# Kernel optimization log

Hardware: AMD Instinct MI355X
Metric: run time of the kernel (lower is better)

The kernel has to match this reference:

```python
import jax, jax.numpy as jnp
import numpy as np

N_EMBD = 1024
N_HEAD = 16
HEAD_DIM = N_EMBD // N_HEAD


def setup_inputs() -> dict:
    key = jax.random.key(0)
    k1, k2, k3, k4, k5 = jax.random.split(key, 5)
    x = jax.random.normal(k1, (4, 2048, N_EMBD), dtype=jnp.float32)
    s = 1.0 / np.sqrt(N_EMBD)
    W_attn = jax.random.normal(k2, (N_EMBD, 3 * N_EMBD), dtype=jnp.float32) * s
    b_attn = jnp.zeros((3 * N_EMBD,), dtype=jnp.float32)
    W_proj = jax.random.normal(k3, (N_EMBD, N_EMBD), dtype=jnp.float32) * s
    b_proj = jnp.zeros((N_EMBD,), dtype=jnp.float32)
    return {"x": x, "W_attn": W_attn, "b_attn": b_attn, "W_proj": W_proj, "b_proj": b_proj}


def _attention(x, W_attn, b_attn, W_proj, b_proj):
    B, T, C = x.shape
    qkv = jnp.einsum("btc,cd->btd", x, W_attn) + b_attn  # [B,T,3C]
    q, k, v = jnp.split(qkv, 3, axis=-1)
    # [B,T,C] -> [B,H,T,D]
    def heads(t):
        return t.reshape(B, T, N_HEAD, HEAD_DIM).transpose(0, 2, 1, 3)
    q, k, v = heads(q), heads(k), heads(v)
    scale = 1.0 / np.sqrt(HEAD_DIM)
    scores = jnp.einsum("bhqd,bhkd->bhqk", q, k) * scale  # [B,H,T,T]
    causal = jnp.tril(jnp.ones((T, T), dtype=bool))
    scores = jnp.where(causal, scores, jnp.finfo(scores.dtype).min)
    attn = jax.nn.softmax(scores, axis=-1)
    y = jnp.einsum("bhqk,bhkd->bhqd", attn, v)  # [B,H,T,D]
    y = y.transpose(0, 2, 1, 3).reshape(B, T, C)
    return jnp.einsum("btc,cd->btd", y, W_proj) + b_proj


def reference(x, W_attn, b_attn, W_proj, b_proj):
    return _attention(x, W_attn, b_attn, W_proj, b_proj)
```

## Files before the change

kernel.cpp:

```cpp
#include <hip/hip_runtime.h>
#include <hip/hip_bf16.h>

#define BB 4
#define TT 2048
#define CC 1024
#define HH 16
#define DD 64
#define BT (BB*TT)
#define C3 (3*CC)
#define LDST 72
#define QSCALE 0.18033688011112042f

typedef __attribute__((ext_vector_type(8))) short short8;
typedef __attribute__((ext_vector_type(4))) float f32x4;

__device__ __forceinline__ short f2bs(float f) {
  __hip_bfloat16 h = __float2bfloat16(f);
  return *reinterpret_cast<short*>(&h);
}

__device__ __forceinline__ void gl_lds16(const short* g, short* l) {
  __builtin_amdgcn_global_load_lds(
      (const __attribute__((address_space(1))) void*)(g),
      (__attribute__((address_space(3))) void*)(l), 16, 0, 0);
}

__global__ __launch_bounds__(256)
void prep(const float* __restrict__ Wa, short* __restrict__ Wat,
          const float* __restrict__ Wp, short* __restrict__ Wpt,
          const float* __restrict__ x, short* __restrict__ Xb)
{
  __shared__ float Lt[64][65];
  const int bx = blockIdx.x;
  if (bx >= 64) {
    size_t chunk = (size_t)(bx - 64) * 16 + blockIdx.y;
    size_t i = (chunk * 256 + threadIdx.x) * 8;
    float4 a = *reinterpret_cast<const float4*>(x + i);
    float4 b = *reinterpret_cast<const float4*>(x + i + 4);
    short8 o;
    o[0] = f2bs(a.x); o[1] = f2bs(a.y); o[2] = f2bs(a.z); o[3] = f2bs(a.w);
    o[4] = f2bs(b.x); o[5] = f2bs(b.y); o[6] = f2bs(b.z); o[7] = f2bs(b.w);
    *reinterpret_cast<short8*>(Xb + i) = o;
    return;
  }
  const bool isA = (bx < 48);
  const float* in  = isA ? Wa  : Wp;
  short*       out = isA ? Wat : Wpt;
  const int N  = isA ? C3 : CC;
  const int n0 = (isA ? bx : bx - 48) * 64;
  const int k0 = blockIdx.y * 64;
  const int cx = threadIdx.x & 15, rr = threadIdx.x >> 4;
#pragma unroll
  for (int p = 0; p < 4; ++p) {
    int kr = p * 16 + rr;
    float4 u = *reinterpret_cast<const float4*>(in + (size_t)(k0 + kr) * N + n0 + cx * 4);
    Lt[kr][cx * 4 + 0] = u.x;
    Lt[kr][cx * 4 + 1] = u.y;
    Lt[kr][cx * 4 + 2] = u.z;
    Lt[kr][cx * 4 + 3] = u.w;
  }
  __syncthreads();
#pragma unroll
  for (int p = 0; p < 4; ++p) {
    int nr = p * 16 + rr;
    short4 o;
    o.x = f2bs(Lt[cx * 4 + 0][nr]);
    o.y = f2bs(Lt[cx * 4 + 1][nr]);
    o.z = f2bs(Lt[cx * 4 + 2][nr]);
    o.w = f2bs(Lt[cx * 4 + 3][nr]);
    *reinterpret_cast<short4*>(out + (size_t)(n0 + nr) * CC + k0 + cx * 4) = o;
  }
}

template<bool QKV>
__global__ __launch_bounds__(512, 2)
void gemm256(const short* __restrict__ A, const short* __restrict__ Bt,
             const float* __restrict__ bias,
             short* __restrict__ qb, short* __restrict__ kb, short* __restrict__ vb,
             float* __restrict__ out)
{
  __shared__ __align__(16) short As[2][2 * 256 * 32];
  __shared__ __align__(16) short Bs[2][2 * 256 * 32];

  const int t = threadIdx.x;
  const int lane = t & 63;
  const int l16 = lane & 15, quad = lane >> 4;
  const int w = t >> 6;
  const int wr = w >> 2, wc = w & 3;

  const int per   = gridDim.x >> 3;
  const int chunk = (blockIdx.x & 7) * per + (blockIdx.x >> 3);
  const int NBC   = QKV ? 12 : 4;
  const int brow  = chunk / NBC, bcol = chunk % NBC;
  const int row0  = brow * 256;
  const int col0  = bcol * 256;

  auto stageHalf = [&](int b, int kc, int ktile) {
#pragma unroll
    for (int q = 0; q < 2; ++q) {
      int gq = (w * 2 + q) * 64 + lane;
      int rq = gq >> 2;
      int cs = ((gq & 3) ^ (rq & 3)) << 3;
      gl_lds16(A  + (size_t)(row0 + rq) * CC + ktile * 64 + kc * 32 + cs,
               &As[b][kc * 8192 + gq * 8]);
      gl_lds16(Bt + (size_t)(col0 + rq) * CC + ktile * 64 + kc * 32 + cs,
               &Bs[b][kc * 8192 + gq * 8]);
    }
  };

  f32x4 acc[8][4];
#pragma unroll
  for (int i = 0; i < 8; ++i)
#pragma unroll
    for (int j = 0; j < 4; ++j) acc[i][j] = (f32x4){0.f, 0.f, 0.f, 0.f};

  stageHalf(0, 0, 0);
  stageHalf(0, 1, 0);

  for (int kt = 0; kt < 16; ++kt) {
    const int cur = kt & 1;
    const short* Ac = As[cur];
    const short* Bc = Bs[cur];
#pragma unroll
    for (int kc = 0; kc < 2; ++kc) {
      if (kt == 15 && kc == 1) {
        asm volatile("s_waitcnt vmcnt(0)" ::: "memory");
      } else {
        asm volatile("s_waitcnt vmcnt(4)" ::: "memory");
      }
      __builtin_amdgcn_s_barrier();
      __builtin_amdgcn_sched_barrier(0);

      short8 af[8], bf[4];
#pragma unroll
      for (int j = 0; j < 4; ++j) {
        int rb = wc * 64 + j * 16 + l16;
        bf[j] = *reinterpret_cast<const short8*>(
            &Bc[kc * 8192 + rb * 32 + (((quad ^ rb) & 3) << 3)]);
      }
#pragma unroll
      for (int i = 0; i < 8; ++i) {
        int ra = wr * 128 + i * 16 + l16;
        af[i] = *reinterpret_cast<const short8*>(
            &Ac[kc * 8192 + ra * 32 + (((quad ^ ra) & 3) << 3)]);
      }

      if (kt < 15) stageHalf(cur ^ 1, kc, kt + 1);

      __builtin_amdgcn_s_setprio(1);
#pragma unroll
      for (int i = 0; i < 8; ++i)
#pragma unroll
        for (int j = 0; j < 4; ++j)
          acc[i][j] = __builtin_amdgcn_mfma_f32_16x16x32_bf16(af[i], bf[j], acc[i][j], 0, 0, 0);
      __builtin_amdgcn_s_setprio(0);
    }
  }

  if constexpr (QKV) {
#pragma unroll
    for (int j = 0; j < 4; ++j) {
      int colb = col0 + wc * 64 + j * 16 + l16;
      int sel  = colb >> 10, cin = colb & 1023;
      int h    = cin >> 6,  dd  = cin & 63;
      float bv = bias[colb];
#pragma unroll
      for (int i = 0; i < 8; ++i)
#pragma unroll
        for (int r = 0; r < 4; ++r) {
          int row = row0 + wr * 128 + i * 16 + quad * 4 + r;
          int bi = row >> 11, tt = row & 2047;
          float val = acc[i][j][r] + bv;
          size_t hb = (size_t)(bi * HH + h);
          if (sel == 0) {
            qb[(hb * TT + tt) * DD + dd] = f2bs(val * QSCALE);
          } else if (sel == 1) {
            kb[(hb * TT + tt) * DD + dd] = f2bs(val);
          } else {
            int tp = (tt & ~63) | (((tt & 15) << 2) | ((tt >> 4) & 3));
            vb[(hb * DD + dd) * TT + tp] = f2bs(val);
          }
        }
    }
  } else {
#pragma unroll
    for (int j = 0; j < 4; ++j) {
      int col = col0 + wc * 64 + j * 16 + l16;
      float bv = bias[col];
#pragma unroll
      for (int i = 0; i < 8; ++i)
#pragma unroll
        for (int r = 0; r < 4; ++r) {
          int row = row0 + wr * 128 + i * 16 + quad * 4 + r;
          out[(size_t)row * CC + col] = acc[i][j][r] + bv;
        }
    }
  }
}

__global__ __launch_bounds__(256, 4)
void attn_mfma(const short* __restrict__ Qb, const short* __restrict__ Kb,
               const short* __restrict__ Vb, short* __restrict__ Y)
{
  __shared__ __align__(16) short Ks[64 * LDST];
  __shared__ __align__(16) short Vt[64 * LDST];
  __shared__ __align__(16) short Pw[4 * 16 * LDST];

  const int t    = threadIdx.x;
  const int w    = t >> 6;
  const int lane = t & 63;
  const int l16  = lane & 15;
  const int quad = lane >> 4;

  const int linear = blockIdx.x + 16 * (blockIdx.y + 16 * blockIdx.z);
  const int nb  = (linear & 7) * 128 + (linear >> 3);
  const int qt0 = nb & 15;
  const int h   = (nb >> 4) & 15;
  const int bi  = nb >> 8;
  const size_t head = (size_t)(bi * HH + h) * TT * DD;

  short* myP = &Pw[w * 16 * LDST];
  const int sr = t >> 2;
  const int sc = (t & 3) << 4;

  const int qts[2] = { qt0, 31 - qt0 };

#pragma unroll
  for (int half = 0; half < 2; ++half) {
    const int qt = qts[half];
    const int q0 = qt * 64;

    short8 qf[2];
#pragma unroll
    for (int kc = 0; kc < 2; ++kc)
      qf[kc] = *reinterpret_cast<const short8*>(
          &Qb[head + (size_t)(q0 + w * 16 + l16) * DD + kc * 32 + quad * 8]);

    f32x4 O[4];
#pragma unroll
    for (int dt = 0; dt < 4; ++dt) O[dt] = (f32x4){0.f, 0.f, 0.f, 0.f};
    float lsum[4] = {};

    for (int kt = 0; kt <= qt; ++kt) {
      const int k0 = kt * 64;
      __syncthreads();

      {
        const short* kg = Kb + head + (size_t)(k0 + sr) * DD + sc;
        short8 a = *reinterpret_cast<const short8*>(kg);
        short8 b = *reinterpret_cast<const short8*>(kg + 8);
        *reinterpret_cast<short8*>(&Ks[sr * LDST + sc])     = a;
        *reinterpret_cast<short8*>(&Ks[sr * LDST + sc + 8]) = b;
        const short* vg = Vb + head + (size_t)sr * TT + k0 + sc;
        short8 c = *reinterpret_cast<const short8*>(vg);
        short8 d = *reinterpret_cast<const short8*>(vg + 8);
        *reinterpret_cast<short8*>(&Vt[sr * LDST + sc])     = c;
        *reinterpret_cast<short8*>(&Vt[sr * LDST + sc + 8]) = d;
      }
      __syncthreads();

      short8 kf[4][2];
#pragma unroll
      for (int nt = 0; nt < 4; ++nt)
#pragma unroll
        for (int kc = 0; kc < 2; ++kc)
          kf[nt][kc] = *reinterpret_cast<const short8*>(
              &Ks[(nt * 16 + l16) * LDST + kc * 32 + quad * 8]);

      f32x4 s[4];
#pragma unroll
      for (int nt = 0; nt < 4; ++nt) s[nt] = (f32x4){0.f, 0.f, 0.f, 0.f};
#pragma unroll
      for (int nt = 0; nt < 4; ++nt)
#pragma unroll
        for (int kc = 0; kc < 2; ++kc)
          s[nt] = __builtin_amdgcn_mfma_f32_16x16x32_bf16(qf[kc], kf[nt][kc], s[nt], 0, 0, 0);

      const int rowg_base = q0 + w * 16 + quad * 4;
#pragma unroll
      for (int r = 0; r < 4; ++r) {
        const int rowg = rowg_base + r;
        short pk[4];
#pragma unroll
        for (int nt = 0; nt < 4; ++nt) {
          float e = (k0 + nt * 16 + l16 <= rowg) ? __builtin_amdgcn_exp2f(s[nt][r]) : 0.f;
          lsum[r] += e;
          pk[nt] = f2bs(e);
        }
        short4 p4; p4.x = pk[0]; p4.y = pk[1]; p4.z = pk[2]; p4.w = pk[3];
        *reinterpret_cast<short4*>(&myP[(quad * 4 + r) * LDST + (l16 << 2)]) = p4;
      }

#pragma unroll
      for (int cc = 0; cc < 2; ++cc) {
        short8 pf = *reinterpret_cast<const short8*>(
            &myP[l16 * LDST + cc * 32 + quad * 8]);
#pragma unroll
        for (int dt = 0; dt < 4; ++dt) {
          short8 vf = *reinterpret_cast<const short8*>(
              &Vt[(dt * 16 + l16) * LDST + cc * 32 + quad * 8]);
          O[dt] = __builtin_amdgcn_mfma_f32_16x16x32_bf16(pf, vf, O[dt], 0, 0, 0);
        }
      }
    }

    float linv[4];
#pragma unroll
    for (int r = 0; r < 4; ++r) {
      float s = lsum[r];
      s += __shfl_xor(s, 1);
      s += __shfl_xor(s, 2);
      s += __shfl_xor(s, 4);
      s += __shfl_xor(s, 8);
      linv[r] = 1.f / s;
    }
#pragma unroll
    for (int dt = 0; dt < 4; ++dt)
#pragma unroll
      for (int r = 0; r < 4; ++r) {
        int tg = q0 + w * 16 + quad * 4 + r;
        Y[((size_t)bi * TT + tg) * CC + h * DD + dt * 16 + l16] =
            f2bs(O[dt][r] * linv[r]);
      }
  }
}

extern "C" void kernel_launch(void* const* d_in, const int* in_sizes, int n_in,
                              void* d_out, int out_size, void* d_ws, size_t ws_size,
                              hipStream_t stream) {
  const float* x  = (const float*)d_in[0];
  const float* Wa = (const float*)d_in[1];
  const float* ba = (const float*)d_in[2];
  const float* Wp = (const float*)d_in[3];
  const float* bp = (const float*)d_in[4];
  float* out = (float*)d_out;

  const size_t NELT = (size_t)BB * HH * TT * DD;
  short* qb  = (short*)d_ws;
  short* kb  = qb + NELT;
  short* vb  = kb + NELT;
  short* Xb  = vb + NELT;
  short* Wat = Xb  + (size_t)BT * CC;
  short* Wpt = Wat + (size_t)CC * C3;
  short* Yb  = Wpt + (size_t)CC * CC;

  prep<<<dim3(64 + 256, 16), 256, 0, stream>>>(Wa, Wat, Wp, Wpt, x, Xb);

  gemm256<true> <<<dim3((C3 / 256) * (BT / 256)), 512, 0, stream>>>(Xb, Wat, ba, qb, kb, vb, nullptr);
  attn_mfma     <<<dim3(16, HH, BB),              256, 0, stream>>>(qb, kb, vb, Yb);
  gemm256<false><<<dim3((CC / 256) * (BT / 256)), 512, 0, stream>>>(Yb, Wpt, bp, nullptr, nullptr, nullptr, out);
}
```

Measured before the change: 285.7 us.

## Restructure GEMM main loop into finer-grained four-phase pipeline with new LDS swizzle

The bf16 GEMM main loop is rewritten into four phases per K tile. Each phase loads half of the A fragments and issues a quarter of the next tiles' global-to-LDS copies, and the loads are prefetched two half-tiles ahead with explicit vmcnt waits and double barriers. The LDS XOR swizzle changes to use row>>1, aimed at reducing bank conflicts for the 16-byte reads. The attention kernel also wraps its MFMA blocks in s_setprio to favour matrix issue. The aim is to overlap global loads with MFMA work and lower register pressure, at the cost of more barriers per tile and a tighter correctness dependence on the wait counts.

After: 283.8 us. No clear change (-0.7%).

```diff
diff --git a/kernel.cpp b/kernel.cpp
--- a/kernel.cpp
+++ b/kernel.cpp
@@ -95,16 +95,19 @@
   const int row0  = brow * 256;
   const int col0  = bcol * 256;
 
-  auto stageHalf = [&](int b, int kc, int ktile) {
-#pragma unroll
-    for (int q = 0; q < 2; ++q) {
-      int gq = (w * 2 + q) * 64 + lane;
+  auto stageQ = [&](int bufS, int kcS, int tileS, bool isA) {
+#pragma unroll
+    for (int l = 0; l < 2; ++l) {
+      int gq = l * 512 + t;
       int rq = gq >> 2;
-      int cs = ((gq & 3) ^ (rq & 3)) << 3;
-      gl_lds16(A  + (size_t)(row0 + rq) * CC + ktile * 64 + kc * 32 + cs,
-               &As[b][kc * 8192 + gq * 8]);
-      gl_lds16(Bt + (size_t)(col0 + rq) * CC + ktile * 64 + kc * 32 + cs,
-               &Bs[b][kc * 8192 + gq * 8]);
+      int g  = (gq & 3) ^ ((rq >> 1) & 3);
+      if (isA) {
+        gl_lds16(A + (size_t)(row0 + rq) * CC + tileS * 64 + kcS * 32 + g * 8,
+                 &As[bufS][kcS * 8192 + gq * 8]);
+      } else {
+        gl_lds16(Bt + (size_t)(col0 + rq) * CC + tileS * 64 + kcS * 32 + g * 8,
+                 &Bs[bufS][kcS * 8192 + gq * 8]);
+      }
     }
   };
 
@@ -114,46 +117,64 @@
 #pragma unroll
     for (int j = 0; j < 4; ++j) acc[i][j] = (f32x4){0.f, 0.f, 0.f, 0.f};
 
-  stageHalf(0, 0, 0);
-  stageHalf(0, 1, 0);
-
-  for (int kt = 0; kt < 16; ++kt) {
-    const int cur = kt & 1;
-    const short* Ac = As[cur];
-    const short* Bc = Bs[cur];
-#pragma unroll
-    for (int kc = 0; kc < 2; ++kc) {
-      if (kt == 15 && kc == 1) {
-        asm volatile("s_waitcnt vmcnt(0)" ::: "memory");
-      } else {
-        asm volatile("s_waitcnt vmcnt(4)" ::: "memory");
-      }
+  stageQ(0, 0, 0, true);  stageQ(0, 0, 0, false);
+  stageQ(0, 1, 0, true);  stageQ(0, 1, 0, false);
+  stageQ(1, 0, 1, true);  stageQ(1, 0, 1, false);
+  asm volatile("s_waitcnt vmcnt(8)" ::: "memory");
+  __builtin_amdgcn_s_barrier();
+
+#pragma unroll
+  for (int u = 0; u < 16; ++u) {
+    const int cb = u & 1;
+    const short* Ac = As[cb];
+    const short* Bc = Bs[cb];
+    short8 bf[4];
+#pragma unroll
+    for (int ph = 0; ph < 4; ++ph) {
+      const int kc = ph >> 1, q = ph & 1;
+
+      if (q == 0) {
+#pragma unroll
+        for (int j = 0; j < 4; ++j) {
+          int rb = wc * 64 + j * 16 + l16;
+          bf[j] = *reinterpret_cast<const short8*>(
+              &Bc[kc * 8192 + rb * 32 + (((quad ^ (rb >> 1)) & 3) << 3)]);
+        }
+      }
+      short8 af[4];
+#pragma unroll
+      for (int iq = 0; iq < 4; ++iq) {
+        int ra = wr * 128 + (q * 4 + iq) * 16 + l16;
+        af[iq] = *reinterpret_cast<const short8*>(
+            &Ac[kc * 8192 + ra * 32 + (((quad ^ (ra >> 1)) & 3) << 3)]);
+      }
+
+      if      (ph == 0) { if (u < 15) stageQ((u + 1) & 1, 1, u + 1, true ); }
+      else if (ph == 1) { if (u < 15) stageQ((u + 1) & 1, 1, u + 1, false); }
+      else if (ph == 2) { if (u < 14) stageQ(u & 1,       0, u + 2, true ); }
+      else              { if (u < 14) stageQ(u & 1,       0, u + 2, false); }
+
       __builtin_amdgcn_s_barrier();
+      asm volatile("s_waitcnt lgkmcnt(0)" ::: "memory");
       __builtin_amdgcn_sched_barrier(0);
 
-      short8 af[8], bf[4];
-#pragma unroll
-      for (int j = 0; j < 4; ++j) {
-        int rb = wc * 64 + j * 16 + l16;
-        bf[j] = *reinterpret_cast<const short8*>(
-            &Bc[kc * 8192 + rb * 32 + (((quad ^ rb) & 3) << 3)]);
-      }
-#pragma unroll
-      for (int i = 0; i < 8; ++i) {
-        int ra = wr * 128 + i * 16 + l16;
-        af[i] = *reinterpret_cast<const short8*>(
-            &Ac[kc * 8192 + ra * 32 + (((quad ^ ra) & 3) << 3)]);
-      }
-
-      if (kt < 15) stageHalf(cur ^ 1, kc, kt + 1);
-
       __builtin_amdgcn_s_setprio(1);
 #pragma unroll
-      for (int i = 0; i < 8; ++i)
+      for (int iq = 0; iq < 4; ++iq)
 #pragma unroll
         for (int j = 0; j < 4; ++j)
-          acc[i][j] = __builtin_amdgcn_mfma_f32_16x16x32_bf16(af[i], bf[j], acc[i][j], 0, 0, 0);
+          acc[q * 4 + iq][j] =
+              __builtin_amdgcn_mfma_f32_16x16x32_bf16(af[iq], bf[j], acc[q * 4 + iq][j], 0, 0, 0);
       __builtin_amdgcn_s_setprio(0);
+
+      if (ph == 1) {
+        if (u == 15)      { asm volatile("s_waitcnt vmcnt(0)" ::: "memory"); }
+        else              { asm volatile("s_waitcnt vmcnt(8)" ::: "memory"); }
+      } else if (ph == 3) {
+        if (u < 14)       { asm volatile("s_waitcnt vmcnt(8)" ::: "memory"); }
+        else if (u == 14) { asm volatile("s_waitcnt vmcnt(4)" ::: "memory"); }
+      }
+      __builtin_amdgcn_s_barrier();
     }
   }
 
@@ -270,11 +291,13 @@
       f32x4 s[4];
 #pragma unroll
       for (int nt = 0; nt < 4; ++nt) s[nt] = (f32x4){0.f, 0.f, 0.f, 0.f};
+      __builtin_amdgcn_s_setprio(1);
 #pragma unroll
       for (int nt = 0; nt < 4; ++nt)
 #pragma unroll
         for (int kc = 0; kc < 2; ++kc)
           s[nt] = __builtin_amdgcn_mfma_f32_16x16x32_bf16(qf[kc], kf[nt][kc], s[nt], 0, 0, 0);
+      __builtin_amdgcn_s_setprio(0);
 
       const int rowg_base = q0 + w * 16 + quad * 4;
 #pragma unroll
@@ -291,6 +314,7 @@
         *reinterpret_cast<short4*>(&myP[(quad * 4 + r) * LDST + (l16 << 2)]) = p4;
       }
 
+      __builtin_amdgcn_s_setprio(1);
 #pragma unroll
       for (int cc = 0; cc < 2; ++cc) {
         short8 pf = *reinterpret_cast<const short8*>(
@@ -302,6 +326,7 @@
           O[dt] = __builtin_amdgcn_mfma_f32_16x16x32_bf16(pf, vf, O[dt], 0, 0, 0);
         }
       }
+      __builtin_amdgcn_s_setprio(0);
     }
 
     float linv[4];
```
